# Optimization experiments

Hardware: AMD Instinct MI355X
Metric: run time of the kernel (lower is better)

## Reference

```python
import jax, jax.numpy as jnp
import numpy as np

D_MODEL = 1024
D_STATE = 16
D_CONV = 4
EXPAND = 2
D_INNER = D_MODEL * EXPAND
B_SZ = 2
SEQ = 4096


def setup_inputs() -> dict:
    key = jax.random.key(0)
    ks = jax.random.split(key, 11)
    rn = lambda i, shape, scale=1.0: jax.random.normal(ks[i], shape, jnp.float32) * scale
    return {
        "x": rn(0, (B_SZ, SEQ, D_MODEL)),
        "W_in": rn(1, (D_MODEL, D_INNER), D_MODEL ** -0.5),
        "b_in": rn(2, (D_INNER,), 0.01),
        "conv_w": rn(3, (D_INNER, 1, D_CONV), 0.1),   # torch depthwise layout [out_ch, in_ch/groups=1, k]
        "conv_b": rn(4, (D_INNER,), 0.01),
        # A scaled so tanh(A) is contractive -> stable recurrence over 4096 steps
        "A": rn(5, (D_STATE, D_STATE), 0.1),
        "Bp": rn(6, (D_STATE,)),   # B parameter [d_state, 1] flattened
        "Cp": rn(7, (D_STATE,)),   # C parameter [1, d_state] flattened
        "Dp": rn(8, (1,)),
        "W_out": rn(9, (D_INNER, D_MODEL), D_INNER ** -0.5),
        "b_out": rn(10, (D_MODEL,), 0.01),
    }


def reference(x, W_in, b_in, conv_w, conv_b, A, Bp, Cp, Dp, W_out, b_out):
    Bsz, S, _ = x.shape
    d_inner = W_in.shape[1]
    # input projection
    u = x @ W_in + b_in                              # [B, S, d_inner]
    # causal depthwise conv (torch pads k-1 both sides then slices [:S])
    u = u.transpose(0, 2, 1)                         # [B, d_inner, S]
    u = jax.lax.conv_general_dilated(
        u, conv_w, window_strides=(1,), padding=[(D_CONV - 1, 0)],
        dimension_numbers=("NCH", "OIH", "NCH"),
        feature_group_count=d_inner) + conv_b[None, :, None]
    u = u.transpose(0, 2, 1)                         # [B, S, d_inner]
    # per-channel scalar SSM shared across channels: h_t = tanh(A) h_{t-1} + B u_t; y_t = C h_t + D u_t
    At = jnp.tanh(A)                                 # [ds, ds]
    def step(h, u_t):                                # h: [B, d_inner, ds], u_t: [B, d_inner]
        h = jnp.einsum("ij,bdj->bdi", At, h) + u_t[..., None] * Bp
        y = jnp.einsum("j,bdj->bd", Cp, h) + Dp[0] * u_t
        return h, y
    h0 = jnp.zeros((Bsz, d_inner, Bp.shape[0]), x.dtype)
    _, ys = jax.lax.scan(step, h0, u.transpose(1, 0, 2))  # ys: [S, B, d_inner]
    y = jax.nn.silu(ys.transpose(1, 0, 2))           # [B, S, d_inner]
    return y @ W_out + b_out                         # [B, S, d_model]
```

## Files before the change

kernel.cpp:

```cpp
#include <hip/hip_runtime.h>

typedef unsigned short u16;
typedef float  f32x4  __attribute__((ext_vector_type(4)));
typedef __bf16 bf16x8 __attribute__((ext_vector_type(8)));
typedef u16    u16x2  __attribute__((ext_vector_type(2)));
typedef u16    u16x4  __attribute__((ext_vector_type(4)));

#define D_MODEL 1024
#define D_INNER 2048
#define B_SZ    2
#define SEQ     4096
#define MROWS   (B_SZ * SEQ)
#define LTAPS   32
#define AW      96
#define VROW    104

__device__ __forceinline__ u16 f2bf(float f) {
    return __builtin_bit_cast(u16, (__bf16)f);
}
__device__ __forceinline__ float bf2f(u16 h) {
    unsigned u = ((unsigned)h) << 16;
    return __builtin_bit_cast(float, u);
}

typedef __attribute__((address_space(1))) void gv_t;
typedef __attribute__((address_space(3))) void lv_t;
__device__ __forceinline__ void glds16(const u16* g, u16* l) {
    __builtin_amdgcn_global_load_lds((gv_t*)g, (lv_t*)l, 16, 0, 0);
}
#define WAIT_VM(n) (0x0F70 | (n))
#define WAIT_LGKM0 0xC07F

__device__ __forceinline__ void transpose_tile(
    const float* __restrict__ in, u16* __restrict__ out,
    int R, int C, int c0, int r0, int tid, float (*tile)[33])
{
    const int tx = tid & 31, ty = tid >> 5;
    for (int k = 0; k < 32; k += 8)
        tile[ty + k][tx] = in[(size_t)(r0 + ty + k) * C + c0 + tx];
    __syncthreads();
    for (int k = 0; k < 32; k += 8)
        out[(size_t)(c0 + ty + k) * R + r0 + tx] = f2bf(tile[tx][ty + k]);
}

__global__ __launch_bounds__(256) void prep_kernel(
    const float* __restrict__ x, u16* __restrict__ xb,
    const float* __restrict__ Win, u16* __restrict__ WinT,
    const float* __restrict__ Wout, u16* __restrict__ WoutT,
    const float* __restrict__ A, const float* __restrict__ Bp,
    const float* __restrict__ Cp, const float* __restrict__ Dp,
    u16* __restrict__ Amat32)
{
    __shared__ float tile[32][33];
    __shared__ float fs[LTAPS];
    const int bx = blockIdx.x, tid = threadIdx.x;
    if (bx < 8192) {
        size_t i = ((size_t)bx * 256 + tid) * 4;
        f32x4 v = *(const f32x4*)(x + i);
        u16x4 o;
        o.x = f2bf(v.x); o.y = f2bf(v.y); o.z = f2bf(v.z); o.w = f2bf(v.w);
        *(u16x4*)(xb + i) = o;
    } else if (bx < 10240) {
        const int flat = bx - 8192;
        transpose_tile(Win, WinT, 1024, 2048,
                       (flat & 63) * 32, (flat >> 6) * 32, tid, tile);
    } else if (bx < 12288) {
        const int flat = bx - 10240;
        transpose_tile(Wout, WoutT, 2048, 1024,
                       (flat & 31) * 32, (flat >> 5) * 32, tid, tile);
    } else {
        if (tid < 64) {
            const int i = tid & 15;
            float Atr[16];
            for (int j = 0; j < 16; j++) Atr[j] = tanhf(A[i * 16 + j]);
            float p = Bp[i];
            const float c  = Cp[i];
            const float d0 = Dp[0];
            for (int t = 0; t < LTAPS; t++) {
                float fv = c * p;
                fv += __shfl_xor(fv, 1); fv += __shfl_xor(fv, 2);
                fv += __shfl_xor(fv, 4); fv += __shfl_xor(fv, 8);
                if (tid == 0) fs[t] = fv + (t == 0 ? d0 : 0.f);
                float n0 = 0.f, n1 = 0.f, n2 = 0.f, n3 = 0.f;
                #pragma unroll
                for (int j = 0; j < 4; j++) {
                    n0 = fmaf(Atr[j],      __shfl(p, j),      n0);
                    n1 = fmaf(Atr[j + 4],  __shfl(p, j + 4),  n1);
                    n2 = fmaf(Atr[j + 8],  __shfl(p, j + 8),  n2);
                    n3 = fmaf(Atr[j + 12], __shfl(p, j + 12), n3);
                }
                p = (n0 + n1) + (n2 + n3);
            }
        }
        __syncthreads();
        for (int idx = tid; idx < 64 * AW; idx += 256) {
            const int i = idx / AW, j = idx - i * AW;
            const int tau = LTAPS + i - j;
            float v = (tau >= 0 && tau < LTAPS) ? fs[tau] : 0.f;
            Amat32[idx] = f2bf(v);
        }
    }
}

template <int BM, int BN, int WM, int WN, int MODE>
__global__ __launch_bounds__(512, 2) void gemm_k1_kernel(
    const u16* __restrict__ Ain, const u16* __restrict__ BT,
    void* __restrict__ Cout, const float* __restrict__ bias,
    int N, int K)
{
    constexpr int FM = BM / WM / 16, FN = BN / WN / 16;
    constexpr int SBU = (BM + BN) * 32;
    constexpr int AGL = BM / 128, BGL = BN / 128;
    constexpr int LGL = AGL + BGL;
    static_assert(WM * WN == 8, "8 waves");
    __shared__ __align__(16) u16 sm[4 * SBU];
    const int tid = threadIdx.x, lane = tid & 63, wid = tid >> 6;
    const int bid = blockIdx.x;
    const int xcd = bid & 7, loc = bid >> 3;
    const int mt = xcd * 4 + (loc & 3), nt = loc >> 2;
    const int m0 = mt * BM, n0 = nt * BN;
    const int wm = wid % WM, wn = wid / WM;
    const int fr = lane & 15, fq = lane >> 4;

    auto mk = [&](const u16* G, int r0, int q) -> const u16* {
        const int l = q ^ (((q >> 7) & 7) << 4);
        return G + (size_t)(r0 + (l >> 6)) * K + ((l & 63) >> 1);
    };
    const u16* pA[AGL];
    const u16* pB[BGL];
    #pragma unroll
    for (int j = 0; j < AGL; ++j) pA[j] = mk(Ain, m0, tid * 16 + j * 8192);
    #pragma unroll
    for (int j = 0; j < BGL; ++j) pB[j] = mk(BT, n0, tid * 16 + j * 8192);

    auto stage = [&](int t) {
        u16* sb = sm + (t & 3) * SBU;
        #pragma unroll
        for (int j = 0; j < AGL; ++j)
            glds16(pA[j] + t * 32, sb + tid * 8 + j * 4096);
        #pragma unroll
        for (int j = 0; j < BGL; ++j)
            glds16(pB[j] + t * 32, sb + BM * 32 + tid * 8 + j * 4096);
    };

    int aoff[FM], boff[FN];
    #pragma unroll
    for (int mi = 0; mi < FM; ++mi) {
        const int la = (wm * (BM / WM) + mi * 16 + fr) * 64 + fq * 16;
        aoff[mi] = (la ^ (((la >> 7) & 7) << 4)) >> 1;
    }
    #pragma unroll
    for (int ni = 0; ni < FN; ++ni) {
        const int lb = (wn * (BN / WN) + ni * 16 + fr) * 64 + fq * 16;
        boff[ni] = ((lb ^ (((lb >> 7) & 7) << 4)) >> 1) + BM * 32;
    }

    f32x4 acc[FM][FN] = {};
    const int NT = K >> 5;

    stage(0); stage(1);
    asm volatile("" ::: "memory");
    __builtin_amdgcn_s_waitcnt(WAIT_VM(LGL));
    __builtin_amdgcn_sched_barrier(0);
    __builtin_amdgcn_s_barrier();

#define K1_PHASE(p, DOSTAGE, WVM)                                            \
  {                                                                          \
    const u16* sb_ = sm + ((p) & 3) * SBU;                                   \
    bf16x8 af[FM], bfr[FN];                                                  \
    _Pragma("unroll")                                                        \
    for (int mi = 0; mi < FM; ++mi)                                          \
      af[mi] = *(const bf16x8*)(sb_ + aoff[mi]);                             \
    _Pragma("unroll")                                                        \
    for (int ni = 0; ni < FN; ++ni)                                          \
      bfr[ni] = *(const bf16x8*)(sb_ + boff[ni]);                            \
    if (DOSTAGE) stage((p) + 2);                                             \
    asm volatile("" ::: "memory");                                           \
    __builtin_amdgcn_sched_barrier(0);                                       \
    __builtin_amdgcn_s_barrier();                                            \
    __builtin_amdgcn_s_waitcnt(WAIT_LGKM0);                                  \
    __builtin_amdgcn_sched_barrier(0);                                       \
    __builtin_amdgcn_s_setprio(1);                                           \
    _Pragma("unroll")                                                        \
    for (int mi = 0; mi < FM; ++mi)                                          \
      _Pragma("unroll")                                                      \
      for (int ni = 0; ni < FN; ++ni)                                        \
        acc[mi][ni] = __builtin_amdgcn_mfma_f32_16x16x32_bf16(               \
            bfr[ni], af[mi], acc[mi][ni], 0, 0, 0);                          \
    __builtin_amdgcn_s_setprio(0);                                           \
    if ((WVM) >= 0) {                                                        \
      asm volatile("" ::: "memory");                                         \
      __builtin_amdgcn_s_waitcnt(WAIT_VM(WVM));                              \
      __builtin_amdgcn_sched_barrier(0);                                     \
      __builtin_amdgcn_s_barrier();                                          \
    }                                                                        \
  }

    #pragma unroll 1
    for (int p = 0; p < NT - 2; ++p)
        K1_PHASE(p, true, LGL)
    K1_PHASE(NT - 2, false, 0)
    K1_PHASE(NT - 1, false, -1)
#undef K1_PHASE

    #pragma unroll
    for (int ni = 0; ni < FN; ++ni) {
        const int colb = n0 + wn * (BN / WN) + ni * 16 + fq * 4;
        const f32x4 bv = *(const f32x4*)(bias + colb);
        #pragma unroll
        for (int mi = 0; mi < FM; ++mi) {
            const int row = m0 + wm * (BM / WM) + mi * 16 + fr;
            f32x4 v = acc[mi][ni];
            v.x += bv.x; v.y += bv.y; v.z += bv.z; v.w += bv.w;
            if constexpr (MODE == 0) {
                u16x4 o;
                o.x = f2bf(v.x); o.y = f2bf(v.y); o.z = f2bf(v.z); o.w = f2bf(v.w);
                *(u16x4*)((u16*)Cout + (size_t)row * N + colb) = o;
            } else {
                *(f32x4*)((float*)Cout + (size_t)row * N + colb) = v;
            }
        }
    }
}

__global__ __launch_bounds__(256) void conv_fir_mfma_kernel(
    const u16* __restrict__ u, const float* __restrict__ cw,
    const float* __restrict__ cb, const u16* __restrict__ Amat32,
    u16* __restrict__ Y)
{
    __shared__ u16 VT[128 * VROW];
    const int tid = threadIdx.x;
    const int c0 = blockIdx.x * 128, t0 = blockIdx.y * 64, b = blockIdx.z;
    {
        const int tx = tid & 63, ty = tid >> 6;
        const int cg = c0 + tx * 2;
        const f32x4 wA = *(const f32x4*)(cw + cg * 4);
        const f32x4 wB = *(const f32x4*)(cw + cg * 4 + 4);
        const float cb0 = cb[cg], cb1 = cb[cg + 1];
        const u16* ucol = u + (size_t)b * SEQ * D_INNER + cg;
        u16* vr0 = VT + (tx * 2)     * VROW;
        u16* vr1 = VT + (tx * 2 + 1) * VROW;

        auto conv_run = [&](int s0, int idx0, int NJ) {
            float am3 = 0.f, am2 = 0.f, am1 = 0.f;
            float bm3 = 0.f, bm2 = 0.f, bm1 = 0.f;
            if (s0 > 0) {
                u16x2 d3 = *(const u16x2*)(ucol + (size_t)(s0 - 3) * D_INNER);
                u16x2 d2 = *(const u16x2*)(ucol + (size_t)(s0 - 2) * D_INNER);
                u16x2 d1 = *(const u16x2*)(ucol + (size_t)(s0 - 1) * D_INNER);
                am3 = bf2f(d3.x); bm3 = bf2f(d3.y);
                am2 = bf2f(d2.x); bm2 = bf2f(d2.y);
                am1 = bf2f(d1.x); bm1 = bf2f(d1.y);
            }
            #pragma unroll 2
            for (int j = 0; j < NJ; j++) {
                const u16* p = ucol + (size_t)(s0 + j * 4) * D_INNER;
                u16x2 r0 = *(const u16x2*)(p);
                u16x2 r1 = *(const u16x2*)(p + (size_t)D_INNER);
                u16x2 r2 = *(const u16x2*)(p + (size_t)2 * D_INNER);
                u16x2 r3 = *(const u16x2*)(p + (size_t)3 * D_INNER);
                float a0 = bf2f(r0.x), b0 = bf2f(r0.y);
                float a1 = bf2f(r1.x), b1 = bf2f(r1.y);
                float a2 = bf2f(r2.x), b2 = bf2f(r2.y);
                float a3 = bf2f(r3.x), b3 = bf2f(r3.y);
                u16x4 oa, ob;
                oa.x = f2bf(cb0 + wA.x * am3 + wA.y * am2 + wA.z * am1 + wA.w * a0);
                oa.y = f2bf(cb0 + wA.x * am2 + wA.y * am1 + wA.z * a0  + wA.w * a1);
                oa.z = f2bf(cb0 + wA.x * am1 + wA.y * a0  + wA.z * a1  + wA.w * a2);
                oa.w = f2bf(cb0 + wA.x * a0  + wA.y * a1  + wA.z * a2  + wA.w * a3);
                ob.x = f2bf(cb1 + wB.x * bm3 + wB.y * bm2 + wB.z * bm1 + wB.w * b0);
                ob.y = f2bf(cb1 + wB.x * bm2 + wB.y * bm1 + wB.z * b0  + wB.w * b1);
                ob.z = f2bf(cb1 + wB.x * bm1 + wB.y * b0  + wB.z * b1  + wB.w * b2);
                ob.w = f2bf(cb1 + wB.x * b0  + wB.y * b1  + wB.z * b2  + wB.w * b3);
                *(u16x4*)(vr0 + idx0 + j * 4) = oa;
                *(u16x4*)(vr1 + idx0 + j * 4) = ob;
                am3 = a1; am2 = a2; am1 = a3;
                bm3 = b1; bm2 = b2; bm1 = b3;
            }
        };

        if (t0 == 0) {
            u16* zr = VT + (tid >> 1) * VROW + (tid & 1) * 16;
            const u16x4 z = {0, 0, 0, 0};
            #pragma unroll
            for (int j = 0; j < 4; j++) *(u16x4*)(zr + j * 4) = z;
            conv_run(ty * 16, 32 + ty * 16, 4);
        } else {
            conv_run(t0 - 32 + ty * 24, ty * 24, 6);
        }
    }
    __syncthreads();
    const int lane = tid & 63, wid = tid >> 6;
    const int wm = (wid & 1) * 32, wn = (wid >> 1) * 64;
    const int fr = lane & 15, fq = lane >> 4;
    f32x4 acc[2][4] = {};
    #pragma unroll
    for (int kq = 0; kq < 3; kq++) {
        const int k0 = kq * 32;
        bf16x8 af[2], bfr[4];
        #pragma unroll
        for (int mi = 0; mi < 2; mi++)
            af[mi] = *(const bf16x8*)(Amat32 + (wm + mi * 16 + fr) * AW + k0 + fq * 8);
        #pragma unroll
        for (int ni = 0; ni < 4; ni++)
            bfr[ni] = *(const bf16x8*)(VT + (wn + ni * 16 + fr) * VROW + k0 + fq * 8);
        #pragma unroll
        for (int mi = 0; mi < 2; mi++)
            #pragma unroll
            for (int ni = 0; ni < 4; ni++)
                acc[mi][ni] = __builtin_amdgcn_mfma_f32_16x16x32_bf16(
                    bfr[ni], af[mi], acc[mi][ni], 0, 0, 0);
    }
    #pragma unroll
    for (int ni = 0; ni < 4; ni++) {
        const int cbase = c0 + wn + ni * 16 + fq * 4;
        #pragma unroll
        for (int mi = 0; mi < 2; mi++) {
            const int trow = t0 + wm + mi * 16 + fr;
            f32x4 v = acc[mi][ni];
            u16x4 o;
            o.x = f2bf(v.x / (1.f + __expf(-v.x)));
            o.y = f2bf(v.y / (1.f + __expf(-v.y)));
            o.z = f2bf(v.z / (1.f + __expf(-v.z)));
            o.w = f2bf(v.w / (1.f + __expf(-v.w)));
            *(u16x4*)(Y + ((size_t)(b * SEQ + trow)) * D_INNER + cbase) = o;
        }
    }
}

extern "C" void kernel_launch(void* const* d_in, const int* in_sizes, int n_in,
                              void* d_out, int out_size, void* d_ws, size_t ws_size,
                              hipStream_t stream)
{
    const float* x    = (const float*)d_in[0];
    const float* Win  = (const float*)d_in[1];
    const float* bin  = (const float*)d_in[2];
    const float* cw   = (const float*)d_in[3];
    const float* cb   = (const float*)d_in[4];
    const float* A    = (const float*)d_in[5];
    const float* Bp   = (const float*)d_in[6];
    const float* Cp   = (const float*)d_in[7];
    const float* Dp   = (const float*)d_in[8];
    const float* Wout = (const float*)d_in[9];
    const float* bout = (const float*)d_in[10];
    float* out = (float*)d_out;

    char* ws = (char*)d_ws;
    u16* xb     = (u16*)(ws);
    u16* WinT   = (u16*)(ws + 16777216);
    u16* WoutT  = (u16*)(ws + 20971520);
    u16* u      = (u16*)(ws + 25165824);
    u16* Y      = (u16*)(ws + 58720256);
    u16* Amat32 = (u16*)(ws + 92274688);

    prep_kernel<<<12289, 256, 0, stream>>>(x, xb, Win, WinT, Wout, WoutT,
                                           A, Bp, Cp, Dp, Amat32);
    gemm_k1_kernel<256, 256, 2, 4, 0><<<256, 512, 0, stream>>>(
        xb, WinT, u, bin, D_INNER, D_MODEL);
    conv_fir_mfma_kernel<<<dim3(16, 64, 2), 256, 0, stream>>>(u, cw, cb, Amat32, Y);
    gemm_k1_kernel<256, 128, 4, 2, 1><<<256, 512, 0, stream>>>(
        Y, WoutT, out, bout, D_MODEL, D_INNER);
}
```

Baseline: 220.5 us.

## Replace large-tile GEMMs with 128x128 tile, 3-slot pipelined 4-wave kernel

Both projection GEMMs now use a new kernel with 128x128 tiles, 256 threads and three blocks per CU. It replaces the old 256-wide tiles run by 8 waves. The LDS pipeline drops from four buffers to three slots, with the stage for tile t+2 issued before the fragment reads. The per-phase LDS barrier, lgkm wait, sched_barriers and setprio are removed, and K and N become compile-time constants. The aim is more blocks for occupancy and latency hiding and fewer barriers per K step. The cost is less data reuse per tile and more global and LDS traffic.

```diff
diff --git a/kernel.cpp b/kernel.cpp
--- a/kernel.cpp
+++ b/kernel.cpp
@@ -28,8 +28,8 @@
 __device__ __forceinline__ void glds16(const u16* g, u16* l) {
     __builtin_amdgcn_global_load_lds((gv_t*)g, (lv_t*)l, 16, 0, 0);
 }
-#define WAIT_VM(n) (0x0F70 | (n))
-#define WAIT_LGKM0 0xC07F
+#define WAIT_VM4   0x0F74
+#define WAIT_VM0   0x0F70
 
 __device__ __forceinline__ void transpose_tile(
     const float* __restrict__ in, u16* __restrict__ out,
@@ -102,122 +102,106 @@
     }
 }
 
-template <int BM, int BN, int WM, int WN, int MODE>
-__global__ __launch_bounds__(512, 2) void gemm_k1_kernel(
+template <int MODE, int NN, int KK>
+__global__ __launch_bounds__(256, 3) void gemm_t3_kernel(
     const u16* __restrict__ Ain, const u16* __restrict__ BT,
-    void* __restrict__ Cout, const float* __restrict__ bias,
-    int N, int K)
-{
-    constexpr int FM = BM / WM / 16, FN = BN / WN / 16;
-    constexpr int SBU = (BM + BN) * 32;
-    constexpr int AGL = BM / 128, BGL = BN / 128;
-    constexpr int LGL = AGL + BGL;
-    static_assert(WM * WN == 8, "8 waves");
-    __shared__ __align__(16) u16 sm[4 * SBU];
+    void* __restrict__ Cout, const float* __restrict__ bias)
+{
+    constexpr int SLOTU = 8192;
+    constexpr int NT = KK >> 5;
+    __shared__ __align__(16) u16 sm[3 * SLOTU];
     const int tid = threadIdx.x, lane = tid & 63, wid = tid >> 6;
     const int bid = blockIdx.x;
     const int xcd = bid & 7, loc = bid >> 3;
-    const int mt = xcd * 4 + (loc & 3), nt = loc >> 2;
-    const int m0 = mt * BM, n0 = nt * BN;
-    const int wm = wid % WM, wn = wid / WM;
+    const int mt = xcd * 8 + (loc & 7), nt = loc >> 3;
+    const int m0 = mt * 128, n0 = nt * 128;
+    const int wm = wid & 1, wn = wid >> 1;
     const int fr = lane & 15, fq = lane >> 4;
 
     auto mk = [&](const u16* G, int r0, int q) -> const u16* {
         const int l = q ^ (((q >> 7) & 7) << 4);
-        return G + (size_t)(r0 + (l >> 6)) * K + ((l & 63) >> 1);
+        return G + (size_t)(r0 + (l >> 6)) * KK + ((l & 63) >> 1);
     };
-    const u16* pA[AGL];
-    const u16* pB[BGL];
+    const u16* pA0 = mk(Ain, m0, tid * 16);
+    const u16* pA1 = mk(Ain, m0, tid * 16 + 4096);
+    const u16* pB0 = mk(BT, n0, tid * 16);
+    const u16* pB1 = mk(BT, n0, tid * 16 + 4096);
+
+    auto stage = [&](int t, int slot) {
+        u16* sb = sm + slot * SLOTU;
+        const int ko = t * 32;
+        glds16(pA0 + ko, sb + tid * 8);
+        glds16(pA1 + ko, sb + 2048 + tid * 8);
+        glds16(pB0 + ko, sb + 4096 + tid * 8);
+        glds16(pB1 + ko, sb + 6144 + tid * 8);
+    };
+
+    int aoff[4], boff[4];
     #pragma unroll
-    for (int j = 0; j < AGL; ++j) pA[j] = mk(Ain, m0, tid * 16 + j * 8192);
-    #pragma unroll
-    for (int j = 0; j < BGL; ++j) pB[j] = mk(BT, n0, tid * 16 + j * 8192);
-
-    auto stage = [&](int t) {
-        u16* sb = sm + (t & 3) * SBU;
-        #pragma unroll
-        for (int j = 0; j < AGL; ++j)
-            glds16(pA[j] + t * 32, sb + tid * 8 + j * 4096);
-        #pragma unroll
-        for (int j = 0; j < BGL; ++j)
-            glds16(pB[j] + t * 32, sb + BM * 32 + tid * 8 + j * 4096);
-    };
-
-    int aoff[FM], boff[FN];
-    #pragma unroll
-    for (int mi = 0; mi < FM; ++mi) {
-        const int la = (wm * (BM / WM) + mi * 16 + fr) * 64 + fq * 16;
-        aoff[mi] = (la ^ (((la >> 7) & 7) << 4)) >> 1;
-    }
-    #pragma unroll
-    for (int ni = 0; ni < FN; ++ni) {
-        const int lb = (wn * (BN / WN) + ni * 16 + fr) * 64 + fq * 16;
-        boff[ni] = ((lb ^ (((lb >> 7) & 7) << 4)) >> 1) + BM * 32;
-    }
-
-    f32x4 acc[FM][FN] = {};
-    const int NT = K >> 5;
-
-    stage(0); stage(1);
+    for (int i = 0; i < 4; ++i) {
+        const int la = (wm * 64 + i * 16 + fr) * 64 + fq * 16;
+        aoff[i] = (la ^ (((la >> 7) & 7) << 4)) >> 1;
+        const int lb = (wn * 64 + i * 16 + fr) * 64 + fq * 16;
+        boff[i] = ((lb ^ (((lb >> 7) & 7) << 4)) >> 1) + 4096;
+    }
+
+    f32x4 acc[4][4] = {};
+
+    stage(0, 0); stage(1, 1);
     asm volatile("" ::: "memory");
-    __builtin_amdgcn_s_waitcnt(WAIT_VM(LGL));
-    __builtin_amdgcn_sched_barrier(0);
+    __builtin_amdgcn_s_waitcnt(WAIT_VM4);
     __builtin_amdgcn_s_barrier();
-
-#define K1_PHASE(p, DOSTAGE, WVM)                                            \
+    asm volatile("" ::: "memory");
+
+#define T3_PHASE(t, rs, DOSTAGE, WVM)                                        \
   {                                                                          \
-    const u16* sb_ = sm + ((p) & 3) * SBU;                                   \
-    bf16x8 af[FM], bfr[FN];                                                  \
+    if (DOSTAGE) stage((t) + 2, ((rs) + 2 >= 3) ? (rs) - 1 : (rs) + 2);      \
+    const u16* sb_ = sm + (rs) * SLOTU;                                      \
+    bf16x8 af[4], bfr[4];                                                    \
     _Pragma("unroll")                                                        \
-    for (int mi = 0; mi < FM; ++mi)                                          \
-      af[mi] = *(const bf16x8*)(sb_ + aoff[mi]);                             \
+    for (int i = 0; i < 4; ++i) af[i]  = *(const bf16x8*)(sb_ + aoff[i]);    \
     _Pragma("unroll")                                                        \
-    for (int ni = 0; ni < FN; ++ni)                                          \
-      bfr[ni] = *(const bf16x8*)(sb_ + boff[ni]);                            \
-    if (DOSTAGE) stage((p) + 2);                                             \
-    asm volatile("" ::: "memory");                                           \
-    __builtin_amdgcn_sched_barrier(0);                                       \
-    __builtin_amdgcn_s_barrier();                                            \
-    __builtin_amdgcn_s_waitcnt(WAIT_LGKM0);                                  \
-    __builtin_amdgcn_sched_barrier(0);                                       \
-    __builtin_amdgcn_s_setprio(1);                                           \
+    for (int i = 0; i < 4; ++i) bfr[i] = *(const bf16x8*)(sb_ + boff[i]);    \
     _Pragma("unroll")                                                        \
-    for (int mi = 0; mi < FM; ++mi)                                          \
+    for (int mi = 0; mi < 4; ++mi)                                           \
       _Pragma("unroll")                                                      \
-      for (int ni = 0; ni < FN; ++ni)                                        \
+      for (int ni = 0; ni < 4; ++ni)                                         \
         acc[mi][ni] = __builtin_amdgcn_mfma_f32_16x16x32_bf16(               \
             bfr[ni], af[mi], acc[mi][ni], 0, 0, 0);                          \
-    __builtin_amdgcn_s_setprio(0);                                           \
     if ((WVM) >= 0) {                                                        \
       asm volatile("" ::: "memory");                                         \
-      __builtin_amdgcn_s_waitcnt(WAIT_VM(WVM));                              \
-      __builtin_amdgcn_sched_barrier(0);                                     \
+      __builtin_amdgcn_s_waitcnt((WVM) ? WAIT_VM4 : WAIT_VM0);               \
       __builtin_amdgcn_s_barrier();                                          \
+      asm volatile("" ::: "memory");                                         \
     }                                                                        \
   }
 
+    int rs = 0;
     #pragma unroll 1
-    for (int p = 0; p < NT - 2; ++p)
-        K1_PHASE(p, true, LGL)
-    K1_PHASE(NT - 2, false, 0)
-    K1_PHASE(NT - 1, false, -1)
-#undef K1_PHASE
+    for (int t = 0; t < NT - 2; ++t) {
+        T3_PHASE(t, rs, true, 1)
+        rs = (rs == 2) ? 0 : rs + 1;
+    }
+    T3_PHASE(NT - 2, rs, false, 0)
+    rs = (rs == 2) ? 0 : rs + 1;
+    T3_PHASE(NT - 1, rs, false, -1)
+#undef T3_PHASE
 
     #pragma unroll
-    for (int ni = 0; ni < FN; ++ni) {
-        const int colb = n0 + wn * (BN / WN) + ni * 16 + fq * 4;
+    for (int ni = 0; ni < 4; ++ni) {
+        const int colb = n0 + wn * 64 + ni * 16 + fq * 4;
         const f32x4 bv = *(const f32x4*)(bias + colb);
         #pragma unroll
-        for (int mi = 0; mi < FM; ++mi) {
-            const int row = m0 + wm * (BM / WM) + mi * 16 + fr;
+        for (int mi = 0; mi < 4; ++mi) {
+            const int row = m0 + wm * 64 + mi * 16 + fr;
             f32x4 v = acc[mi][ni];
             v.x += bv.x; v.y += bv.y; v.z += bv.z; v.w += bv.w;
             if constexpr (MODE == 0) {
                 u16x4 o;
                 o.x = f2bf(v.x); o.y = f2bf(v.y); o.z = f2bf(v.z); o.w = f2bf(v.w);
-                *(u16x4*)((u16*)Cout + (size_t)row * N + colb) = o;
+                *(u16x4*)((u16*)Cout + (size_t)row * NN + colb) = o;
             } else {
-                *(f32x4*)((float*)Cout + (size_t)row * N + colb) = v;
+                *(f32x4*)((float*)Cout + (size_t)row * NN + colb) = v;
             }
         }
     }
@@ -355,9 +339,9 @@
 
     prep_kernel<<<12289, 256, 0, stream>>>(x, xb, Win, WinT, Wout, WoutT,
                                            A, Bp, Cp, Dp, Amat32);
-    gemm_k1_kernel<256, 256, 2, 4, 0><<<256, 512, 0, stream>>>(
-        xb, WinT, u, bin, D_INNER, D_MODEL);
+    gemm_t3_kernel<0, D_INNER, D_MODEL><<<1024, 256, 0, stream>>>(
+        xb, WinT, u, bin);
     conv_fir_mfma_kernel<<<dim3(16, 64, 2), 256, 0, stream>>>(u, cw, cb, Amat32, Y);
-    gemm_k1_kernel<256, 128, 4, 2, 1><<<256, 512, 0, stream>>>(
-        Y, WoutT, out, bout, D_MODEL, D_INNER);
-}
+    gemm_t3_kernel<1, D_MODEL, D_INNER><<<512, 256, 0, stream>>>(
+        Y, WoutT, out, bout);
+}
```

Result: no change. 224.1 us (+1.6%).

## Restructure GEMM main loop to process two K-subtiles per single barrier

Applied to the files above, without the earlier changes.

The GEMM pipeline moves from one barrier pair per 32-wide K step to one barrier per 64-wide step. Each step waits for all outstanding loads, issues async loads for the next two subtiles, then runs MFMAs over the two current subtiles in the 4-slot LDS ring. This halves the synchronisation points, but each step now waits on all in-flight loads (vmcnt 0), so the prefetch distance is shorter. Launch bounds also drop from 2 to 1 blocks per CU, which changes register allocation limits.

```diff
diff --git a/kernel.cpp b/kernel.cpp
--- a/kernel.cpp
+++ b/kernel.cpp
@@ -28,8 +28,7 @@
 __device__ __forceinline__ void glds16(const u16* g, u16* l) {
     __builtin_amdgcn_global_load_lds((gv_t*)g, (lv_t*)l, 16, 0, 0);
 }
-#define WAIT_VM(n) (0x0F70 | (n))
-#define WAIT_LGKM0 0xC07F
+#define WAIT_VM0   0x0F70
 
 __device__ __forceinline__ void transpose_tile(
     const float* __restrict__ in, u16* __restrict__ out,
@@ -103,7 +102,7 @@
 }
 
 template <int BM, int BN, int WM, int WN, int MODE>
-__global__ __launch_bounds__(512, 2) void gemm_k1_kernel(
+__global__ __launch_bounds__(512, 1) void gemm_f_kernel(
     const u16* __restrict__ Ain, const u16* __restrict__ BT,
     void* __restrict__ Cout, const float* __restrict__ bias,
     int N, int K)
@@ -111,7 +110,6 @@
     constexpr int FM = BM / WM / 16, FN = BN / WN / 16;
     constexpr int SBU = (BM + BN) * 32;
     constexpr int AGL = BM / 128, BGL = BN / 128;
-    constexpr int LGL = AGL + BGL;
     static_assert(WM * WN == 8, "8 waves");
     __shared__ __align__(16) u16 sm[4 * SBU];
     const int tid = threadIdx.x, lane = tid & 63, wid = tid >> 6;
@@ -133,14 +131,14 @@
     #pragma unroll
     for (int j = 0; j < BGL; ++j) pB[j] = mk(BT, n0, tid * 16 + j * 8192);
 
-    auto stage = [&](int t) {
-        u16* sb = sm + (t & 3) * SBU;
+    auto stage_sub = [&](int s) {
+        u16* sb = sm + (s & 3) * SBU;
         #pragma unroll
         for (int j = 0; j < AGL; ++j)
-            glds16(pA[j] + t * 32, sb + tid * 8 + j * 4096);
+            glds16(pA[j] + s * 32, sb + tid * 8 + j * 4096);
         #pragma unroll
         for (int j = 0; j < BGL; ++j)
-            glds16(pB[j] + t * 32, sb + BM * 32 + tid * 8 + j * 4096);
+            glds16(pB[j] + s * 32, sb + BM * 32 + tid * 8 + j * 4096);
     };
 
     int aoff[FM], boff[FN];
@@ -156,52 +154,39 @@
     }
 
     f32x4 acc[FM][FN] = {};
-    const int NT = K >> 5;
-
-    stage(0); stage(1);
-    asm volatile("" ::: "memory");
-    __builtin_amdgcn_s_waitcnt(WAIT_VM(LGL));
-    __builtin_amdgcn_sched_barrier(0);
-    __builtin_amdgcn_s_barrier();
-
-#define K1_PHASE(p, DOSTAGE, WVM)                                            \
-  {                                                                          \
-    const u16* sb_ = sm + ((p) & 3) * SBU;                                   \
-    bf16x8 af[FM], bfr[FN];                                                  \
-    _Pragma("unroll")                                                        \
-    for (int mi = 0; mi < FM; ++mi)                                          \
-      af[mi] = *(const bf16x8*)(sb_ + aoff[mi]);                             \
-    _Pragma("unroll")                                                        \
-    for (int ni = 0; ni < FN; ++ni)                                          \
-      bfr[ni] = *(const bf16x8*)(sb_ + boff[ni]);                            \
-    if (DOSTAGE) stage((p) + 2);                                             \
-    asm volatile("" ::: "memory");                                           \
-    __builtin_amdgcn_sched_barrier(0);                                       \
-    __builtin_amdgcn_s_barrier();                                            \
-    __builtin_amdgcn_s_waitcnt(WAIT_LGKM0);                                  \
-    __builtin_amdgcn_sched_barrier(0);                                       \
-    __builtin_amdgcn_s_setprio(1);                                           \
-    _Pragma("unroll")                                                        \
-    for (int mi = 0; mi < FM; ++mi)                                          \
-      _Pragma("unroll")                                                      \
-      for (int ni = 0; ni < FN; ++ni)                                        \
-        acc[mi][ni] = __builtin_amdgcn_mfma_f32_16x16x32_bf16(               \
-            bfr[ni], af[mi], acc[mi][ni], 0, 0, 0);                          \
-    __builtin_amdgcn_s_setprio(0);                                           \
-    if ((WVM) >= 0) {                                                        \
-      asm volatile("" ::: "memory");                                         \
-      __builtin_amdgcn_s_waitcnt(WAIT_VM(WVM));                              \
-      __builtin_amdgcn_sched_barrier(0);                                     \
-      __builtin_amdgcn_s_barrier();                                          \
-    }                                                                        \
-  }
+    const int NT = K >> 6;
+
+    stage_sub(0); stage_sub(1);
 
     #pragma unroll 1
-    for (int p = 0; p < NT - 2; ++p)
-        K1_PHASE(p, true, LGL)
-    K1_PHASE(NT - 2, false, 0)
-    K1_PHASE(NT - 1, false, -1)
-#undef K1_PHASE
+    for (int t = 0; t < NT; ++t) {
+        asm volatile("" ::: "memory");
+        __builtin_amdgcn_s_waitcnt(WAIT_VM0);
+        __builtin_amdgcn_sched_barrier(0);
+        __builtin_amdgcn_s_barrier();
+        __builtin_amdgcn_sched_barrier(0);
+        if (t + 1 < NT) { stage_sub(2 * t + 2); stage_sub(2 * t + 3); }
+        asm volatile("" ::: "memory");
+        __builtin_amdgcn_s_setprio(1);
+        #pragma unroll
+        for (int kh = 0; kh < 2; ++kh) {
+            const u16* sb_ = sm + ((2 * t + kh) & 3) * SBU;
+            bf16x8 af[FM], bfr[FN];
+            #pragma unroll
+            for (int mi = 0; mi < FM; ++mi)
+                af[mi] = *(const bf16x8*)(sb_ + aoff[mi]);
+            #pragma unroll
+            for (int ni = 0; ni < FN; ++ni)
+                bfr[ni] = *(const bf16x8*)(sb_ + boff[ni]);
+            #pragma unroll
+            for (int mi = 0; mi < FM; ++mi)
+                #pragma unroll
+                for (int ni = 0; ni < FN; ++ni)
+                    acc[mi][ni] = __builtin_amdgcn_mfma_f32_16x16x32_bf16(
+                        bfr[ni], af[mi], acc[mi][ni], 0, 0, 0);
+        }
+        __builtin_amdgcn_s_setprio(0);
+    }
 
     #pragma unroll
     for (int ni = 0; ni < FN; ++ni) {
@@ -355,9 +340,9 @@
 
     prep_kernel<<<12289, 256, 0, stream>>>(x, xb, Win, WinT, Wout, WoutT,
                                            A, Bp, Cp, Dp, Amat32);
-    gemm_k1_kernel<256, 256, 2, 4, 0><<<256, 512, 0, stream>>>(
+    gemm_f_kernel<256, 256, 2, 4, 0><<<256, 512, 0, stream>>>(
         xb, WinT, u, bin, D_INNER, D_MODEL);
     conv_fir_mfma_kernel<<<dim3(16, 64, 2), 256, 0, stream>>>(u, cw, cb, Amat32, Y);
-    gemm_k1_kernel<256, 128, 4, 2, 1><<<256, 512, 0, stream>>>(
+    gemm_f_kernel<256, 128, 4, 2, 1><<<256, 512, 0, stream>>>(
         Y, WoutT, out, bout, D_MODEL, D_INNER);
 }
```

Measured after the change: 223.1 us. No clear change (+1.2%).
